# Kernel optimization log

Hardware: AMD Instinct MI355X
Metric: run time of the kernel (lower is better)

## Reference

```python
import jax, jax.numpy as jnp
import numpy as np

B, N, D, H = 8, 1024, 768, 4
ALPHA = 0.2      # LeakyReLU negative slope in GraphAttentionLayer
NEG = -9e15      # mask fill value for non-edges (pyGAT convention)


def setup_inputs() -> dict:
    key = jax.random.key(0)
    ks = jax.random.split(key, 8)
    input_emb = jax.random.normal(ks[0], (B, N, D), jnp.float32)
    adj = jax.random.randint(ks[1], (B, N, N), 0, 2, dtype=jnp.int32)
    mask_node = jnp.ones((B, N), jnp.float32)
    s = 1.0 / np.sqrt(D).astype(np.float32)
    W_heads = jax.random.normal(ks[2], (H, D, D), jnp.float32) * s          # per-head W: nfeat->nhid
    a_heads = jax.random.normal(ks[3], (H, 2 * D, 1), jnp.float32) * s      # per-head attention vector a
    W_out = jax.random.normal(ks[4], (H * D, D), jnp.float32) * (1.0 / np.sqrt(H * D).astype(np.float32))
    a_out = jax.random.normal(ks[5], (2 * D, 1), jnp.float32) * s
    w_cls = jax.random.normal(ks[6], (D, 1), jnp.float32) * s               # Classifier.linear1 weight
    b_cls = jnp.zeros((1,), jnp.float32)
    return dict(input_emb=input_emb, adj=adj, mask_node=mask_node,
                W_heads=W_heads, a_heads=a_heads, W_out=W_out, a_out=a_out,
                w_cls=w_cls, b_cls=b_cls)


def _gat_layer(x, adj_mask, W, a, concat):
    # x: [B,N,Fin], W: [Fin,Fout], a: [2*Fout,1], adj_mask: [B,N,N] bool
    Wh = jnp.einsum('bnd,df->bnf', x, W)            # [B,N,Fout]
    Fo = W.shape[1]
    f1 = Wh @ a[:Fo]                                 # [B,N,1] source term
    f2 = Wh @ a[Fo:]                                 # [B,N,1] target term
    e = jax.nn.leaky_relu(f1 + jnp.swapaxes(f2, 1, 2), ALPHA)  # [B,N,N]
    e = jnp.where(adj_mask, e, NEG)
    att = jax.nn.softmax(e, axis=-1)                 # dropout=0 -> no attention dropout
    h = jnp.einsum('bij,bjf->bif', att, Wh)          # [B,N,Fout]
    return jax.nn.elu(h) if concat else h


def reference(input_emb, adj, mask_node, W_heads, a_heads, W_out, a_out, w_cls, b_cls):
    adj_mask = adj > 0
    # multi-head GAT (concat=True heads), vectorized over heads and batch
    heads = jax.vmap(lambda Wi, ai: _gat_layer(input_emb, adj_mask, Wi, ai, True))(W_heads, a_heads)  # [H,B,N,D]
    xx = jnp.moveaxis(heads, 0, 2).reshape(B, N, H * D)  # torch.cat over heads, dim=1 per node
    out = jax.nn.elu(_gat_layer(xx, adj_mask, W_out, a_out, False))
    # dropout_layer(p=0.5) assumed eval mode (identity); residual add
    yy = out + input_emb                               # [B,N,D]
    h = (yy @ w_cls + b_cls)[..., 0]                   # Classifier linear -> [B,N]
    node_scores = jax.nn.sigmoid(h) * mask_node
    return yy, node_scores
```

## Files before the change

### kernel.cpp

```cpp
#include <hip/hip_runtime.h>


typedef unsigned short ushortT;
typedef _Float16 f16;
typedef __attribute__((ext_vector_type(8))) _Float16 f16x8;
typedef __attribute__((ext_vector_type(4))) _Float16 f16x4;
typedef __attribute__((ext_vector_type(4))) float f32x4;
typedef __attribute__((ext_vector_type(2))) float f32x2;
typedef __attribute__((ext_vector_type(8))) unsigned short u16x8;
typedef __attribute__((ext_vector_type(2))) unsigned short u16x2;
typedef __attribute__((ext_vector_type(4))) int i32x4;

#define ALPHA 0.2f

__device__ __forceinline__ float b2f(ushortT u) {
  union { unsigned int i; float f; } c; c.i = ((unsigned int)u) << 16; return c.f;
}
__device__ __forceinline__ ushortT f2b(float f) {
  union { float f; unsigned int u; } c; c.f = f;
  unsigned int u = c.u;
  u += 0x7FFFu + ((u >> 16) & 1u);
  return (ushortT)(u >> 16);
}
__device__ __forceinline__ f16* whB(char* dout, int flg) {
  return (f16*)(dout + (flg ? 22020096L : 11010048L));
}
__device__ __forceinline__ float* fbuf(int sel, float* Pws, char* dout, int flg) {
  if (sel == 0) return Pws;
  return (float*)(dout + (flg ? 25165824L : 12582912L) + (long)(sel - 1) * 8192);
}
__device__ __forceinline__ void gld16(const f16* g, f16* l) {
  __builtin_amdgcn_global_load_lds(
      (const __attribute__((address_space(1))) void*)g,
      (__attribute__((address_space(3))) void*)l, 16, 0, 0);
}

__global__ void detect_dtype(const ushortT* __restrict__ X, int* __restrict__ flag,
                             float* __restrict__ Pws, char* __restrict__ dout) {
  __shared__ int s[256];
  int t = threadIdx.x, c = 0;
  for (int i = t; i < 16384; i += 256) {
    int e = (X[2 * i] >> 7) & 0xFF;
    if (e > 140 || e < 100) c++;
  }
  s[t] = c; __syncthreads();
  for (int o = 128; o > 0; o >>= 1) { if (t < o) s[t] += s[t + o]; __syncthreads(); }
  __syncthreads();
  int fl = (s[0] > 1000) ? 1 : 0;
  if (t == 0) *flag = fl;
  float* Qv = (float*)(dout + (fl ? 25165824L : 12582912L));
#pragma unroll
  for (int i = 0; i < 8; i++) Pws[t + i * 256] = 0.f;
#pragma unroll
  for (int i = 0; i < 16; i++) Qv[t + i * 256] = 0.f;
}

struct GA {
  const void* A; const void* B; void* C; const void* R; const void* avec;
  long aOff, bOff, cOff, rOff, avOff;
  int K, lda, ldb, aRaw, accum, fd, fsel, zmask, bWhb, cWhb;
};

template <int MODE, int BSRC>
__device__ void gbody(const GA a, float* Pws, char* dout, int flg,
                      f16* AS, f16* BS, int n0, int m0, bool bid0) {
  int t = threadIdx.x;
  int aTy = a.aRaw ? (flg ? 2 : 1) : 0;
  float* fv = fbuf(a.fsel, Pws, dout, flg);
  const void* Bres = a.bWhb ? (const void*)whB(dout, flg) : a.B;
  void*       Cres = a.cWhb ? (void*)whB(dout, flg) : a.C;

  if (a.zmask && bid0) {
#pragma unroll
    for (int sb = 0; sb < 3; sb++)
      if ((a.zmask >> sb) & 1) {
        float* z = fbuf(sb, Pws, dout, flg);
#pragma unroll
        for (int i = 0; i < 8; i++) z[t + i * 256] = 0.f;
      }
  }

  const f16*     Ah = (const f16*)a.A;
  const ushortT* Au = (const ushortT*)a.A;
  const float*   Af = (const float*)a.A;
  const f16*     Bh = (const f16*)Bres;
  const ushortT* Bu = (const ushortT*)Bres;
  const float*   Bf = (const float*)Bres;

  int lane = t & 63, wid = t >> 6;
  int wr = wid >> 1, wc = wid & 1;
  int lr = lane & 15, lg = lane >> 4, l7 = lane & 7;
  int aRow0 = (wr * 32 + lr) * 64, aRow1 = aRow0 + 16 * 64;
  int bRow0 = (wc * 32 + lr) * 64, bRow1 = bRow0 + 16 * 64;
  int ch0 = ((lg) ^ l7) * 8, ch1 = ((4 + lg) ^ l7) * 8;

  f32x4 acc[2][2];
#pragma unroll
  for (int i = 0; i < 2; i++)
#pragma unroll
    for (int j = 0; j < 2; j++) acc[i][j] = (f32x4){0.f, 0.f, 0.f, 0.f};

  auto compute = [&](int cur) {
    f16* Ac = AS + cur * 4096; f16* Bc = BS + cur * 4096;
#pragma unroll
    for (int kk = 0; kk < 2; kk++) {
      int ch = kk ? ch1 : ch0;
      f16x8 a0 = *(const f16x8*)(Ac + aRow0 + ch);
      f16x8 a1 = *(const f16x8*)(Ac + aRow1 + ch);
      f16x8 b0 = *(const f16x8*)(Bc + bRow0 + ch);
      f16x8 b1 = *(const f16x8*)(Bc + bRow1 + ch);
      acc[0][0] = __builtin_amdgcn_mfma_f32_16x16x32_f16(a0, b0, acc[0][0], 0, 0, 0);
      acc[0][1] = __builtin_amdgcn_mfma_f32_16x16x32_f16(a0, b1, acc[0][1], 0, 0, 0);
      acc[1][0] = __builtin_amdgcn_mfma_f32_16x16x32_f16(a1, b0, acc[1][0], 0, 0, 0);
      acc[1][1] = __builtin_amdgcn_mfma_f32_16x16x32_f16(a1, b1, acc[1][1], 0, 0, 0);
    }
  };

  int KT = a.K >> 6;

  if (BSRC == 0) {
    int gr = lane >> 3, gcn = lane & 7, swz = (gcn ^ (gr & 7)) * 8;
    int isB = wid >> 1, cq4 = (wid & 1) * 4;
    long gA = a.aOff + (long)(m0 + gr) * a.lda + swz;
    long gB = a.bOff + (long)(n0 + gr) * (long)a.K + swz;
    auto stageG = [&](int buf, int kt) {
      if (!isB) {
        const f16* g = Ah + gA + (long)kt * 64;
        f16* dst = AS + buf * 4096;
#pragma unroll
        for (int c = 0; c < 4; c++)
          gld16(g + (long)(cq4 + c) * 8 * a.lda, dst + (cq4 + c) * 512);
      } else {
        const f16* g = Bh + gB + (long)kt * 64;
        f16* dst = BS + buf * 4096;
#pragma unroll
        for (int c = 0; c < 4; c++)
          gld16(g + (long)(cq4 + c) * 8 * a.K, dst + (cq4 + c) * 512);
      }
    };
    stageG(0, 0);
    __syncthreads();
    for (int kt = 0; kt < KT; ++kt) {
      int cur = kt & 1;
      if (kt + 1 < KT) stageG(cur ^ 1, kt + 1);
      compute(cur);
      __syncthreads();
    }
  } else {
    int tq = t >> 2, cq = t & 3;
    long aBase = a.aOff + (long)(m0 + tq) * a.lda + cq * 16;
    int stA0 = tq * 64 + (((2 * cq)     ^ (tq & 7)) * 8);
    int stA1 = tq * 64 + (((2 * cq + 1) ^ (tq & 7)) * 8);
    int q2 = t & 31, cB = t >> 5;
    int nb0 = 2 * q2, nb1 = nb0 + 1;
    int stB0 = nb0 * 64 + ((cB ^ (nb0 & 7)) * 8);
    int stB1 = nb1 * 64 + ((cB ^ (nb1 & 7)) * 8);

    f16x8 ra0, ra1, rb0, rb1;
    auto loadA = [&](int kt) {
      long g = aBase + (long)kt * 64;
      if (aTy == 0) {
        ra0 = *(const f16x8*)(Ah + g);
        ra1 = *(const f16x8*)(Ah + g + 8);
      } else if (aTy == 1) {
        u16x8 v0 = *(const u16x8*)(Au + g);
        u16x8 v1 = *(const u16x8*)(Au + g + 8);
#pragma unroll
        for (int j = 0; j < 8; j++) { ra0[j] = (f16)b2f(v0[j]); ra1[j] = (f16)b2f(v1[j]); }
      } else {
        f32x4 v0 = *(const f32x4*)(Af + g);
        f32x4 v1 = *(const f32x4*)(Af + g + 4);
        f32x4 v2 = *(const f32x4*)(Af + g + 8);
        f32x4 v3 = *(const f32x4*)(Af + g + 12);
#pragma unroll
        for (int j = 0; j < 4; j++) {
          ra0[j] = (f16)v0[j]; ra0[4 + j] = (f16)v1[j];
          ra1[j] = (f16)v2[j]; ra1[4 + j] = (f16)v3[j];
        }
      }
    };
    auto loadB = [&](int kt) {
      long rbase = a.bOff + (long)(kt * 64 + cB * 8) * a.ldb + n0 + 2 * q2;
      if (flg) {
#pragma unroll
        for (int j = 0; j < 8; j++) {
          f32x2 v = *(const f32x2*)(Bf + rbase + (long)j * a.ldb);
          rb0[j] = (f16)v[0]; rb1[j] = (f16)v[1];
        }
      } else {
#pragma unroll
        for (int j = 0; j < 8; j++) {
          u16x2 v = *(const u16x2*)(Bu + rbase + (long)j * a.ldb);
          rb0[j] = (f16)b2f(v[0]); rb1[j] = (f16)b2f(v[1]);
        }
      }
    };
    auto stage = [&](int buf) {
      *(f16x8*)(AS + buf * 4096 + stA0) = ra0;
      *(f16x8*)(AS + buf * 4096 + stA1) = ra1;
      *(f16x8*)(BS + buf * 4096 + stB0) = rb0;
      *(f16x8*)(BS + buf * 4096 + stB1) = rb1;
    };
    loadA(0); loadB(0);
    stage(0);
    loadA(1); loadB(1);
    __syncthreads();
    for (int kt = 0; kt < KT; ++kt) {
      int cur = kt & 1;
      if (kt + 1 < KT) stage(cur ^ 1);
      if (kt + 2 < KT) { loadA(kt + 2); loadB(kt + 2); }
      compute(cur);
      __syncthreads();
    }
  }

  int rowb_base = m0 + wr * 32 + 4 * lg;
  int col_base  = n0 + wc * 32 + lr;

  float a1v[2], a2v[2];
  float p1[2][4], p2[2][4];
  if (a.fd) {
    const float* avf = (const float*)a.avec; const ushortT* avu = (const ushortT*)a.avec;
#pragma unroll
    for (int fn = 0; fn < 2; fn++) {
      int c = n0 + wc * 32 + fn * 16 + lr;
      a1v[fn] = flg ? avf[a.avOff + c]       : b2f(avu[a.avOff + c]);
      a2v[fn] = flg ? avf[a.avOff + 768 + c] : b2f(avu[a.avOff + 768 + c]);
    }
#pragma unroll
    for (int fm = 0; fm < 2; fm++)
#pragma unroll
      for (int r = 0; r < 4; r++) { p1[fm][r] = 0.f; p2[fm][r] = 0.f; }
  }

#pragma unroll
  for (int fm = 0; fm < 2; fm++) {
#pragma unroll
    for (int fn = 0; fn < 2; fn++) {
      int rowb = rowb_base + fm * 16;
      int col  = col_base + fn * 16;
      f32x4 v = acc[fm][fn];
      float fullv[4];
      if (MODE == 4) {
        f16x4 pk;
#pragma unroll
        for (int r = 0; r < 4; r++) { fullv[r] = v[r]; pk[r] = (f16)v[r]; }
        *(f16x4*)((f16*)Cres + (long)col * 1024 + rowb) = pk;
      } else if (MODE == 3) {
        f16* Cc = (f16*)Cres;
        long idx = (long)col * 1024 + rowb;
        f16x4 pk;
        if (a.accum) {
          f16x4 old = *(const f16x4*)(Cc + idx);
#pragma unroll
          for (int r = 0; r < 4; r++) { fullv[r] = (float)old[r] + v[r]; pk[r] = (f16)fullv[r]; }
        } else {
#pragma unroll
          for (int r = 0; r < 4; r++) { fullv[r] = v[r]; pk[r] = (f16)v[r]; }
        }
        *(f16x4*)(Cc + idx) = pk;
      } else {
#pragma unroll
        for (int r = 0; r < 4; r++) {
          int row = rowb + r;
          float x = v[r];
          x = x > 0.f ? x : __expf(x) - 1.f;
          long ci = a.cOff + (long)row * 768 + col;
          if (MODE == 2) {
            long ri = a.rOff + (long)row * 768 + col;
            x += flg ? ((const float*)a.R)[ri] : b2f(((const ushortT*)a.R)[ri]);
            if (flg) ((float*)Cres)[ci] = x;
            else     ((ushortT*)Cres)[ci] = f2b(x);
          } else {
            ((f16*)Cres)[ci] = (f16)x;
          }
        }
      }
      if (a.fd) {
        float ac1 = a1v[fn], ac2 = a2v[fn];
#pragma unroll
        for (int r = 0; r < 4; r++) {
          p1[fm][r] += fullv[r] * ac1;
          p2[fm][r] += fullv[r] * ac2;
        }
      }
    }
  }

  if (a.fd) {
#pragma unroll
    for (int fm = 0; fm < 2; fm++)
#pragma unroll
      for (int r = 0; r < 4; r++) {
#pragma unroll
        for (int o = 1; o < 16; o <<= 1) {
          p1[fm][r] += __shfl_xor(p1[fm][r], o);
          p2[fm][r] += __shfl_xor(p2[fm][r], o);
        }
      }
    if (lr == 0) {
#pragma unroll
      for (int fm = 0; fm < 2; fm++)
#pragma unroll
        for (int r = 0; r < 4; r++) {
          int row = rowb_base + fm * 16 + r;
          atomicAdd(fv + row, p1[fm][r]);
          atomicAdd(fv + 1024 + row, p2[fm][r]);
        }
    }
  }
}

__device__ void attn_body(const float* __restrict__ fvb, const int* __restrict__ adj,
                          f16* __restrict__ att, int rowBase) {
  int t = threadIdx.x, lane = t & 63, wid = t >> 6;
  int row = rowBase + wid;
  const float* f2 = fvb + 1024;
  const int* arow = adj + (size_t)row * 1024;
  f16* orow = att + (size_t)row * 1024;
  float f1i = fvb[row];
  int c0 = lane * 16;

  float e[16]; int msk[16];
  float mx = -1e38f;
#pragma unroll
  for (int g = 0; g < 4; g++) {
    i32x4 av = *(const i32x4*)(arow + c0 + g * 4);
    f32x4 fvv = *(const f32x4*)(f2 + c0 + g * 4);
#pragma unroll
    for (int c = 0; c < 4; c++) {
      float ev = f1i + fvv[c];
      ev = ev > 0.f ? ev : ALPHA * ev;
      e[g * 4 + c] = ev;
      msk[g * 4 + c] = av[c] > 0;
      if (msk[g * 4 + c]) mx = fmaxf(mx, ev);
    }
  }
#pragma unroll
  for (int o = 32; o > 0; o >>= 1) mx = fmaxf(mx, __shfl_xor(mx, o));
  bool none = mx < -1e37f;

  float sum = 0.f;
  float p[16];
#pragma unroll
  for (int i = 0; i < 16; i++) {
    p[i] = none ? 1.f : (msk[i] ? __expf(e[i] - mx) : 0.f);
    sum += p[i];
  }
#pragma unroll
  for (int o = 32; o > 0; o >>= 1) sum += __shfl_xor(sum, o);
  float inv = 1.f / sum;
  f16x8 o0, o1;
#pragma unroll
  for (int i = 0; i < 8; i++) { o0[i] = (f16)(p[i] * inv); o1[i] = (f16)(p[8 + i] * inv); }
  *(f16x8*)(orow + c0) = o0;
  *(f16x8*)(orow + c0 + 8) = o1;
}

template <int MODE, int BSRC>
__global__ __launch_bounds__(256) void k_solo(GA a, float* Pws, char* dout,
                                              const int* __restrict__ rflag) {
  __shared__ __align__(16) f16 As[2][4096];
  __shared__ __align__(16) f16 Bs[2][4096];
  gbody<MODE, BSRC>(a, Pws, dout, *rflag, &As[0][0], &Bs[0][0],
                    blockIdx.x * 64, blockIdx.y * 64,
                    blockIdx.x == 0 && blockIdx.y == 0);
}
__global__ __launch_bounds__(256) void k_pairGG(GA g2, GA g1, float* Pws, char* dout,
                                                const int* __restrict__ rflag) {
  __shared__ __align__(16) f16 As[2][4096];
  __shared__ __align__(16) f16 Bs[2][4096];
  int flg = *rflag;
  int id = blockIdx.x;
  if (id < 192)
    gbody<1, 0>(g2, Pws, dout, flg, &As[0][0], &Bs[0][0],
                (id % 12) * 64, (id / 12) * 64, id == 0);
  else {
    int l = id - 192;
    gbody<4, 1>(g1, Pws, dout, flg, &As[0][0], &Bs[0][0],
                (l % 12) * 64, (l / 12) * 64, false);
  }
}
__global__ __launch_bounds__(256) void k_pairGA(GA g3, int rsel,
                                                const int* __restrict__ adj,
                                                f16* __restrict__ att,
                                                float* Pws, char* dout,
                                                const int* __restrict__ rflag) {
  __shared__ __align__(16) f16 As[2][4096];
  __shared__ __align__(16) f16 Bs[2][4096];
  int flg = *rflag;
  int id = blockIdx.x;
  if (id < 192)
    gbody<3, 1>(g3, Pws, dout, flg, &As[0][0], &Bs[0][0],
                (id % 12) * 64, (id / 12) * 64, id == 0);
  else
    attn_body(fbuf(rsel, Pws, dout, flg), adj, att, (id - 192) * 4);
}
__global__ __launch_bounds__(256) void k_attn(int rsel, const int* __restrict__ adj,
                                              f16* __restrict__ att,
                                              float* Pws, char* dout,
                                              const int* __restrict__ rflag) {
  int flg = *rflag;
  attn_body(fbuf(rsel, Pws, dout, flg), adj, att, blockIdx.x * 4);
}

__global__ __launch_bounds__(256) void cls_kernel(
    void* __restrict__ outbase, const void* __restrict__ w,
    const void* __restrict__ bc, const void* __restrict__ mask,
    const int* __restrict__ rflag) {
  int t = threadIdx.x, lane = t & 63, wv = t >> 6;
  long row = (long)blockIdx.x * 4 + wv;
  int f32 = *rflag;
  const float* yf = (const float*)outbase; const ushortT* yu = (const ushortT*)outbase;
  const float* wf = (const float*)w;       const ushortT* wu = (const ushortT*)w;
  float s = 0.f;
  for (int d = lane; d < 768; d += 64) {
    float yv = f32 ? yf[row * 768 + d] : b2f(yu[row * 768 + d]);
    float wvv = f32 ? wf[d] : b2f(wu[d]);
    s += yv * wvv;
  }
#pragma unroll
  for (int o = 32; o > 0; o >>= 1) s += __shfl_down(s, o);
  if (lane == 0) {
    float bb = f32 ? ((const float*)bc)[0] : b2f(((const ushortT*)bc)[0]);
    float mk = f32 ? ((const float*)mask)[row] : b2f(((const ushortT*)mask)[row]);
    float sig = 1.f / (1.f + __expf(-(s + bb)));
    long oi = 6291456L + row;
    if (f32) ((float*)outbase)[oi] = sig * mk;
    else ((ushortT*)outbase)[oi] = f2b(sig * mk);
  }
}

extern "C" void kernel_launch(void* const* d_in, const int* in_sizes, int n_in,
                              void* d_out, int out_size, void* d_ws, size_t ws_size,
                              hipStream_t stream) {
  (void)in_sizes; (void)n_in; (void)out_size; (void)ws_size;

  const void* X    = d_in[0];
  const int*  adj  = (const int*)d_in[1];
  const void* maskN= d_in[2];
  const void* Wh   = d_in[3];
  const void* aH   = d_in[4];
  const void* Wo   = d_in[5];
  const void* aO   = d_in[6];
  const void* wcls = d_in[7];
  const void* bcls = d_in[8];

  char* ws = (char*)d_ws;
  float* Pws  = (float*)(ws + 0);
  int*   flag = (int*)(ws + 8192);
  f16* Wh1A = (f16*)(ws + 8448);
  f16* Wh2T = (f16*)(ws + 1581312);
  f16* attb = (f16*)(ws + 3154176);
  f16* hout = (f16*)(ws + 5251328);
  char* dob = (char*)d_out;

  detect_dtype<<<1, 256, 0, stream>>>((const ushortT*)X, flag, Pws, dob);

  auto mkG1 = [&](int b, int h) {
    GA g{}; g.A = X; g.B = Wh; g.C = Wh1A; g.avec = aH;
    g.aOff = (long)b * 786432; g.bOff = (long)h * 589824;
    g.avOff = (long)h * 1536;
    g.K = 768; g.lda = 768; g.ldb = 768; g.aRaw = 1;
    g.fd = 1; g.cWhb = h & 1;
    return g;
  };
  auto mkG2 = [&](int h) {
    GA g{}; g.A = attb; g.B = Wh1A; g.C = hout;
    g.K = 1024; g.lda = 1024; g.ldb = 1024;
    g.bWhb = h & 1;
    return g;
  };
  auto mkG3 = [&](int h) {
    GA g{}; g.A = hout; g.B = Wo; g.C = Wh2T; g.avec = aO;
    g.bOff = (long)h * 589824;
    g.K = 768; g.lda = 768; g.ldb = 768;
    g.accum = h > 0 ? 1 : 0;
    return g;
  };

  dim3 gg(12, 16);
  int w = 0;
  auto wn = [&]() { int v = w % 3; ++w; return v; };

  int fsG10 = wn();
  {
    GA g1 = mkG1(0, 0); g1.fsel = fsG10;
    k_solo<4, 1><<<gg, 256, 0, stream>>>(g1, Pws, dob, flag);
  }

  for (int b = 0; b < 8; b++) {
    const int* adjb = adj + (size_t)b * 1048576;
    long xOff = (long)b * 786432;

    k_attn<<<256, 256, 0, stream>>>(fsG10, adjb, attb, Pws, dob, flag);

    int lastFsel = 0;
    for (int h = 0; h < 4; h++) {
      GA g2 = mkG2(h);
      bool hasG1 = (h < 3) || (b < 7);
      if (hasG1) {
        int nh = (h < 3) ? h + 1 : 0;
        int nbb = (h < 3) ? b : b + 1;
        GA g1 = mkG1(nbb, nh);
        g1.fsel = wn();
        g2.zmask = (1 << (w % 3)) | ((h == 3) ? (1 << ((w + 1) % 3)) : 0);
        k_pairGG<<<dim3(384), 256, 0, stream>>>(g2, g1, Pws, dob, flag);
        if (nh == 0) fsG10 = g1.fsel;
        lastFsel = g1.fsel;
      } else {
        g2.zmask = (1 << (w % 3));
        k_solo<1, 0><<<gg, 256, 0, stream>>>(g2, Pws, dob, flag);
      }
      if (h < 3) {
        GA g3 = mkG3(h);
        k_pairGA<<<dim3(448), 256, 0, stream>>>(g3, lastFsel, adjb, attb,
                                                Pws, dob, flag);
      }
    }
    GA g33 = mkG3(3); g33.fd = 1; g33.fsel = wn();
    k_solo<3, 1><<<gg, 256, 0, stream>>>(g33, Pws, dob, flag);
    k_attn<<<256, 256, 0, stream>>>(g33.fsel, adjb, attb, Pws, dob, flag);
    GA g4{}; g4.A = attb; g4.B = Wh2T; g4.C = d_out; g4.R = X;
    g4.cOff = xOff; g4.rOff = xOff;
    g4.K = 1024; g4.lda = 1024; g4.ldb = 1024;
    k_solo<2, 0><<<gg, 256, 0, stream>>>(g4, Pws, dob, flag);
  }

  cls_kernel<<<2048, 256, 0, stream>>>(d_out, wcls, bcls, maskN, flag);
}
```

Measured before the change: 1.490 ms.

## Deepen global-to-LDS GEMM pipeline to four buffers with explicit waitcnt barriers

The direct global_load_lds GEMM path now uses four LDS buffers and keeps two tiles in flight, prefetching two steps ahead. __syncthreads is replaced with explicit vmcnt/lgkmcnt waits plus s_barrier and sched_barrier, so the kernel waits only for the oldest tile instead of draining every outstanding load. The register-staged path gets the same explicit lgkmcnt+barrier form. LDS use per block doubles to 64KB, which may lower occupancy, and the hand-counted vmcnt values must match the number of loads issued per stage.

```diff
diff --git a/kernel.cpp b/kernel.cpp
--- a/kernel.cpp
+++ b/kernel.cpp
@@ -13,6 +13,13 @@
 
 #define ALPHA 0.2f
 
+#define VMCNT(n) do { asm volatile("s_waitcnt vmcnt(" #n ")" ::: "memory"); \
+                      __builtin_amdgcn_sched_barrier(0); } while (0)
+#define LGKM0()  do { asm volatile("s_waitcnt lgkmcnt(0)" ::: "memory"); \
+                      __builtin_amdgcn_sched_barrier(0); } while (0)
+#define BARRIER() do { __builtin_amdgcn_s_barrier(); \
+                       __builtin_amdgcn_sched_barrier(0); } while (0)
+
 __device__ __forceinline__ float b2f(ushortT u) {
   union { unsigned int i; float f; } c; c.i = ((unsigned int)u) << 16; return c.f;
 }
@@ -100,8 +107,8 @@
 #pragma unroll
     for (int j = 0; j < 2; j++) acc[i][j] = (f32x4){0.f, 0.f, 0.f, 0.f};
 
-  auto compute = [&](int cur) {
-    f16* Ac = AS + cur * 4096; f16* Bc = BS + cur * 4096;
+  auto compute = [&](int buf) {
+    f16* Ac = AS + buf * 4096; f16* Bc = BS + buf * 4096;
 #pragma unroll
     for (int kk = 0; kk < 2; kk++) {
       int ch = kk ? ch1 : ch0;
@@ -139,12 +146,17 @@
       }
     };
     stageG(0, 0);
-    __syncthreads();
+    stageG(1, 1);
+    VMCNT(4);
+    BARRIER();
     for (int kt = 0; kt < KT; ++kt) {
-      int cur = kt & 1;
-      if (kt + 1 < KT) stageG(cur ^ 1, kt + 1);
-      compute(cur);
-      __syncthreads();
+      if (kt + 2 < KT) stageG((kt + 2) & 3, kt + 2);
+      compute(kt & 3);
+      if (kt + 1 < KT) {
+        if (kt + 2 < KT) { VMCNT(4); } else { VMCNT(0); }
+        LGKM0();
+        BARRIER();
+      }
     }
   } else {
     int tq = t >> 2, cq = t & 3;
@@ -204,13 +216,15 @@
     loadA(0); loadB(0);
     stage(0);
     loadA(1); loadB(1);
-    __syncthreads();
+    LGKM0();
+    BARRIER();
     for (int kt = 0; kt < KT; ++kt) {
       int cur = kt & 1;
       if (kt + 1 < KT) stage(cur ^ 1);
       if (kt + 2 < KT) { loadA(kt + 2); loadB(kt + 2); }
       compute(cur);
-      __syncthreads();
+      LGKM0();
+      BARRIER();
     }
   }
 
@@ -360,16 +374,16 @@
 template <int MODE, int BSRC>
 __global__ __launch_bounds__(256) void k_solo(GA a, float* Pws, char* dout,
                                               const int* __restrict__ rflag) {
-  __shared__ __align__(16) f16 As[2][4096];
-  __shared__ __align__(16) f16 Bs[2][4096];
+  __shared__ __align__(16) f16 As[4][4096];
+  __shared__ __align__(16) f16 Bs[4][4096];
   gbody<MODE, BSRC>(a, Pws, dout, *rflag, &As[0][0], &Bs[0][0],
                     blockIdx.x * 64, blockIdx.y * 64,
                     blockIdx.x == 0 && blockIdx.y == 0);
 }
 __global__ __launch_bounds__(256) void k_pairGG(GA g2, GA g1, float* Pws, char* dout,
                                                 const int* __restrict__ rflag) {
-  __shared__ __align__(16) f16 As[2][4096];
-  __shared__ __align__(16) f16 Bs[2][4096];
+  __shared__ __align__(16) f16 As[4][4096];
+  __shared__ __align__(16) f16 Bs[4][4096];
   int flg = *rflag;
   int id = blockIdx.x;
   if (id < 192)
@@ -386,8 +400,8 @@
                                                 f16* __restrict__ att,
                                                 float* Pws, char* dout,
                                                 const int* __restrict__ rflag) {
-  __shared__ __align__(16) f16 As[2][4096];
-  __shared__ __align__(16) f16 Bs[2][4096];
+  __shared__ __align__(16) f16 As[4][4096];
+  __shared__ __align__(16) f16 Bs[4][4096];
   int flg = *rflag;
   int id = blockIdx.x;
   if (id < 192)
```

Result: no change. 1.476 ms (-1.0%).
